# Kernel tuning notes

Measured on AMD Instinct MI355X. Metric: run time of the kernel, lower is better.

Reference implementation:

```python
import jax, jax.numpy as jnp
import numpy as np

N, B, H, IN_DIM, OUT_DIM = 1024, 16, 64, 2, 12
BACK, STEP = 2.0, 1.0
HIST = int(BACK / STEP)          # history steps = 2
FUR = int(OUT_DIM / STEP)        # future integration steps = 12
THRES = 1e-3                     # edge threshold (thres in __init__)
NBINS = HIST + 1                 # quantized delay bins: 0..HIST steps
N_KNOTS = 11                     # spline intervals (12 knots)


def setup_inputs() -> dict:
    key = jax.random.key(0)
    ks = iter(jax.random.split(key, 32))
    f32 = jnp.float32

    def rn(shape, scale):
        return (scale * jax.random.normal(next(ks), shape, dtype=f32))

    inp = {
        "A": jax.random.uniform(next(ks), (N, N), dtype=f32),
        "all_delay": jax.random.uniform(next(ks), (N, N), dtype=f32) * BACK,
        "coeff_a": rn((B, N, N_KNOTS, IN_DIM), 0.1),
        "coeff_b": rn((B, N, N_KNOTS, IN_DIM), 0.1),
        "coeff_c": rn((B, N, N_KNOTS, IN_DIM), 0.1),
        "coeff_d": rn((B, N, N_KNOTS, IN_DIM), 0.1),
        "node_emb": rn((N, H), 0.1),
        "i2h_W1": rn((IN_DIM, H), 1.0 / np.sqrt(IN_DIM)),
        "i2h_b1": jnp.zeros((H,), f32),
        "i2h_W2": rn((H, H * HIST), 1.0 / np.sqrt(H)),
        "i2h_b2": jnp.zeros((H * HIST,), f32),
        "dde_Wm": rn((H, H), 1.0 / np.sqrt(H)),
        "dde_Ws": rn((H, H), 1.0 / np.sqrt(H)),
        "dde_Wx": rn((IN_DIM, H), 1.0 / np.sqrt(IN_DIM)),
        "dde_b": jnp.zeros((H,), f32),
        "reg_W1": rn((H, H // 2), 1.0 / np.sqrt(H)),
        "reg_b1": jnp.zeros((H // 2,), f32),
        "reg_W2": rn((H // 2, 1), 1.0 / np.sqrt(H // 2)),
        "reg_b2": jnp.zeros((1,), f32),
        "pred_W1": rn((H, H // 2), 1.0 / np.sqrt(H)),
        "pred_b1": jnp.zeros((H // 2,), f32),
        "pred_W2": rn((H // 2, OUT_DIM), 1.0 / np.sqrt(H // 2)),
        "pred_b2": jnp.zeros((OUT_DIM,), f32),
    }
    return inp


def _spline(coeffs, t):
    """Natural cubic spline: value and derivative at scalar time t.
    knots at times BACK + arange(12); coeffs [B,N,11,IN]."""
    a, b, c, d = coeffs
    idx = jnp.clip(jnp.floor(t - BACK).astype(jnp.int32), 0, a.shape[2] - 1)
    frac = t - BACK - idx.astype(a.dtype)
    A_ = jnp.take(a, idx, axis=2)
    B_ = jnp.take(b, idx, axis=2)
    C_ = jnp.take(c, idx, axis=2)
    D_ = jnp.take(d, idx, axis=2)
    val = A_ + frac * (B_ + frac * (C_ + frac * D_))
    der = B_ + frac * (2.0 * C_ + 3.0 * frac * D_)
    return val, der  # each [B,N,IN]


def _forward(A, all_delay, coeff_a, coeff_b, coeff_c, coeff_d, node_emb,
             i2h_W1, i2h_b1, i2h_W2, i2h_b2,
             dde_Wm, dde_Ws, dde_Wx, dde_b,
             reg_W1, reg_b1, reg_W2, reg_b2,
             pred_W1, pred_b1, pred_W2, pred_b2):
    coeffs = (coeff_a, coeff_b, coeff_c, coeff_d)
    # --- dynamic graph build (dense, thresholded) ---
    sem = jax.nn.softmax(jax.nn.relu(node_emb @ node_emb.T), axis=1)     # semantic_A
    Ah = A + jnp.eye(N, dtype=A.dtype)                                   # normalized adj
    dinv = jax.lax.rsqrt(Ah.sum(axis=1))
    spatial = dinv[:, None] * Ah * dinv[None, :]
    Ac = sem + spatial
    W = jnp.where(Ac > THRES, Ac, 0.0)                                   # edge weights
    dsteps = jnp.round(jnp.clip(all_delay, 0.0, BACK) / STEP).astype(jnp.int32)
    Wbins = jnp.stack([jnp.where(dsteps == d, W, 0.0) for d in range(NBINS)])  # [NBINS,N,N]

    # --- history hidden states from initial spline value ---
    x0, _ = _spline(coeffs, jnp.asarray(BACK, A.dtype))                  # [B,N,IN]
    hid = jax.nn.relu(x0 @ i2h_W1 + i2h_b1) @ i2h_W2 + i2h_b2            # [B,N,H*HIST]
    hist = hid.reshape(B, N, HIST, H).transpose(1, 2, 0, 3)              # [N,HIST,B,H]
    S = jnp.concatenate([hist, jnp.zeros((N, FUR, B, H), hist.dtype)], axis=1)
    h0 = hist[:, HIST - 1]                                               # y0 [N,B,H]

    def step(carry, k):
        S, h = carry
        idx = HIST - 1 + k  # current time index in S
        agg = jnp.zeros_like(h)
        for d in range(NBINS):  # delayed message passing per delay bin
            sd = jax.lax.dynamic_slice_in_dim(S, jnp.maximum(idx - d, 0), 1, axis=1)[:, 0]
            agg = agg + jnp.einsum('ji,jbh->ibh', Wbins[d], sd)
        t = BACK + STEP * k.astype(h.dtype)
        _, dx = _spline(coeffs, t)                                       # control derivative
        dx = dx.transpose(1, 0, 2)                                       # [N,B,IN]
        pre = agg @ dde_Wm + h @ dde_Ws + dx @ dde_Wx + dde_b
        h_new = h + STEP * (jnp.tanh(pre) - h)                           # Euler step of DDE
        S = jax.lax.dynamic_update_slice_in_dim(S, h_new[:, None], idx + 1, axis=1)
        return (S, h_new), h_new

    (_, _), y_hidden = jax.lax.scan(step, (S, h0), jnp.arange(FUR))      # [FUR,N,B,H]

    reg = (jax.nn.relu(y_hidden @ reg_W1 + reg_b1) @ reg_W2 + reg_b2)[..., 0]  # [FUR,N,B]
    ts = BACK + jnp.arange(OUT_DIM, dtype=A.dtype)
    tgt = jax.vmap(lambda t: _spline(coeffs, t)[0][:, :, 0].T)(ts)       # [OUT,N,B]
    diff = reg - tgt
    ad = jnp.abs(diff)
    reg_loss = jnp.where(ad < 1.0, 0.5 * diff * diff, ad - 0.5).mean()

    y_pred = (jax.nn.relu(y_hidden[-1] @ pred_W1 + pred_b1) @ pred_W2 + pred_b2)
    y_pred = y_pred.transpose(1, 0, 2)                                   # [B,N,OUT]
    return y_pred, reg_loss


def reference(A, all_delay, coeff_a, coeff_b, coeff_c, coeff_d, node_emb,
              i2h_W1, i2h_b1, i2h_W2, i2h_b2,
              dde_Wm, dde_Ws, dde_Wx, dde_b,
              reg_W1, reg_b1, reg_W2, reg_b2,
              pred_W1, pred_b1, pred_W2, pred_b2):
    return _forward(A, all_delay, coeff_a, coeff_b, coeff_c, coeff_d, node_emb,
                    i2h_W1, i2h_b1, i2h_W2, i2h_b2,
                    dde_Wm, dde_Ws, dde_Wx, dde_b,
                    reg_W1, reg_b1, reg_W2, reg_b2,
                    pred_W1, pred_b1, pred_W2, pred_b2)
```

## Files before the change

kernel.cpp:

```cpp
#include <hip/hip_runtime.h>
#include <cstddef>
#include <cstdint>

#define NN 1024
#define BB 16
#define NKNOTS 11

typedef __attribute__((ext_vector_type(8))) short short8_v;
typedef __attribute__((ext_vector_type(4))) float f32x4;
typedef __attribute__((ext_vector_type(8))) unsigned short ushort8_v;
typedef __attribute__((ext_vector_type(4))) unsigned short ushort4_v;
typedef __attribute__((ext_vector_type(4))) unsigned int uint4_v;
typedef __attribute__((ext_vector_type(2))) unsigned int uint2_v;

#define WPK_OFF   ((size_t)0)
#define M3_OFF    ((size_t)2 << 20)
#define STHI_OFF  ((size_t)6 << 20)
#define STLO_OFF  ((size_t)14 << 20)
#define WGT_OFF   ((size_t)22 << 20)
#define SYNC_OFF  (((size_t)22 << 20) + 16384)
#define LOSS_OFF  (SYNC_OFF + 2048)
#define Z_OFF     (LOSS_OFF + 256)
#define DINV_OFF  (Z_OFF + 4096)

#define AGGS   0
#define AGGH   17408
#define AGGL   25600
#define HH_    33792
#define HL_    41984
#define HT32   50176
#define REDS   66560
#define PL1    68608
#define WGT_L  104448
#define LUT_OFF 120832

__device__ __forceinline__ unsigned short f2bf(float x) {
  unsigned int u = __float_as_uint(x);
  return (unsigned short)((u + 0x7FFFu + ((u >> 16) & 1u)) >> 16);
}
__device__ __forceinline__ float bf2f(unsigned short h) {
  return __uint_as_float(((unsigned int)h) << 16);
}
__device__ __forceinline__ void gload16(const void* g, void* l) {
  __builtin_amdgcn_global_load_lds(
      (const __attribute__((address_space(1))) unsigned int*)g,
      (__attribute__((address_space(3))) unsigned int*)l, 16, 0, 0);
}
__device__ __forceinline__ void gload4(const void* g, void* l) {
  __builtin_amdgcn_global_load_lds(
      (const __attribute__((address_space(1))) unsigned int*)g,
      (__attribute__((address_space(3))) unsigned int*)l, 4, 0, 0);
}

__global__ __launch_bounds__(256) void rowstats_kernel(
    const float* __restrict__ emb, const float* __restrict__ A,
    float* __restrict__ Z, float* __restrict__ dinv)
{
  const int j = blockIdx.x;
  const int tid = threadIdx.x;
  __shared__ float ej[64];
  __shared__ float r1[256], r2[256];
  if (tid < 64) ej[tid] = emb[j * 64 + tid];
  __syncthreads();
  float zs = 0.f, as = 0.f;
  for (int i = tid; i < NN; i += 256) {
    const float4* er = (const float4*)(emb + (size_t)i * 64);
    float dot = 0.f;
#pragma unroll
    for (int q = 0; q < 16; ++q) {
      float4 e = er[q];
      dot += e.x * ej[q * 4 + 0] + e.y * ej[q * 4 + 1] +
             e.z * ej[q * 4 + 2] + e.w * ej[q * 4 + 3];
    }
    zs += expf(fmaxf(dot, 0.f));
    as += A[(size_t)j * NN + i];
  }
  r1[tid] = zs; r2[tid] = as;
  __syncthreads();
  for (int s = 128; s > 0; s >>= 1) {
    if (tid < s) { r1[tid] += r1[tid + s]; r2[tid] += r2[tid + s]; }
    __syncthreads();
  }
  if (tid == 0) {
    Z[j] = r1[0];
    dinv[j] = rsqrtf(r2[0] + 1.0f);
  }
}

__global__ __launch_bounds__(256) void build_wt_kernel(
    const float* __restrict__ emb, const float* __restrict__ A,
    const float* __restrict__ delay, const float* __restrict__ Z,
    const float* __restrict__ dinv,
    unsigned short* __restrict__ Wpk, unsigned int* __restrict__ M3g)
{
  __shared__ float eI[64][65];
  __shared__ float eJ[64][65];
  __shared__ float wS[64][65];
  __shared__ unsigned char dS[64][64];
  __shared__ float diS[64];

  const int tid = threadIdx.x;
  const int it = blockIdx.x >> 4, jt = blockIdx.x & 15;
  const int i0 = it * 64, j0 = jt * 64;

  for (int q = tid; q < 4096; q += 256) {
    int r = q >> 6, c = q & 63;
    eI[r][c] = emb[(size_t)(i0 + r) * 64 + c];
    eJ[r][c] = emb[(size_t)(j0 + r) * 64 + c];
  }
  if (tid < 64) diS[tid] = dinv[i0 + tid];
  __syncthreads();

  const int jj = tid >> 2, iig = (tid & 3) * 16;
  float dotv[16];
#pragma unroll
  for (int m = 0; m < 16; ++m) dotv[m] = 0.f;
#pragma unroll 4
  for (int h4 = 0; h4 < 16; ++h4) {
    float4 a = *(const float4*)&eJ[jj][h4 * 4];
#pragma unroll
    for (int m = 0; m < 16; ++m) {
      float4 bb = *(const float4*)&eI[iig + m][h4 * 4];
      dotv[m] += a.x * bb.x + a.y * bb.y + a.z * bb.z + a.w * bb.w;
    }
  }
  const float Zj = Z[j0 + jj], dj = dinv[j0 + jj];
  const float* Ap = A + (size_t)(j0 + jj) * NN + i0 + iig;
  const float* Dp = delay + (size_t)(j0 + jj) * NN + i0 + iig;
#pragma unroll
  for (int m = 0; m < 16; ++m) {
    float aji = Ap[m] + ((i0 + iig + m) == (j0 + jj) ? 1.f : 0.f);
    float ac = expf(fmaxf(dotv[m], 0.f)) / Zj + dj * diS[iig + m] * aji;
    float w = (ac > 0.001f) ? ac : 0.f;
    float dl = fminf(fmaxf(Dp[m], 0.f), 2.f);
    wS[jj][iig + m] = w;
    dS[jj][iig + m] = (unsigned char)(int)rintf(dl);
  }
  __syncthreads();

  const int iw = tid >> 2, jg = (tid & 3) * 16;
  ushort8_v P0, P1;
#pragma unroll
  for (int m = 0; m < 8; ++m) {
    P0[m] = f2bf(wS[jg + m][iw]);
    P1[m] = f2bf(wS[jg + 8 + m][iw]);
  }
  size_t woff = (size_t)(i0 + iw) * NN + j0 + jg;
  *(ushort8_v*)(Wpk + woff) = P0;
  *(ushort8_v*)(Wpk + woff + 8) = P1;
  uint2_v mw;
#pragma unroll
  for (int o = 0; o < 2; ++o) {
    unsigned int m0 = 0, m1 = 0, m2 = 0;
#pragma unroll
    for (int e = 0; e < 8; ++e) {
      int dv = dS[jg + o * 8 + e][iw];
      m0 |= (dv == 0) << e;
      m1 |= (dv == 1) << e;
      m2 |= (dv == 2) << e;
    }
    mw[o] = m0 | (m1 << 8) | (m2 << 16);
  }
  *(uint2_v*)(M3g + (size_t)(i0 + iw) * 128 + (j0 + jg) / 8) = mw;
}

__global__ __launch_bounds__(256) void init_s_kernel(
    const float* __restrict__ ca, const float* __restrict__ W1,
    const float* __restrict__ b1, const float* __restrict__ W2,
    const float* __restrict__ b2,
    unsigned short* __restrict__ SThi, unsigned short* __restrict__ STlo,
    const float* __restrict__ Wm, const float* __restrict__ Wsm,
    unsigned short* __restrict__ wgt)
{
  const int bid = blockIdx.x;
  const int tid = threadIdx.x;
  if (bid >= 256) {
    int e = (bid - 256) * 256 + tid;
    int n = e >> 7, kk = e & 127;
    float v = (kk < 64) ? Wm[kk * 64 + n] : Wsm[(kk - 64) * 64 + n];
    wgt[n * 128 + (((kk >> 3) ^ (n & 15)) << 3) + (kk & 7)] = f2bf(v);
    return;
  }
  __shared__ float l1S[64][65];
  __shared__ float W2S[64][128];
  __shared__ float hidS[64][129];

  const int nt = bid >> 4, b = bid & 15;
  const int n0 = nt * 64;

  for (int q = tid; q < 2048; q += 256)
    ((float4*)&W2S[0][0])[q] = ((const float4*)W2)[q];

  {
    const int n = tid >> 2, hb = (tid & 3) * 16;
    float2 x = *(const float2*)(ca + ((size_t)(b * NN + n0 + n) * NKNOTS) * 2);
#pragma unroll
    for (int m = 0; m < 16; ++m) {
      int h = hb + m;
      l1S[n][h] = fmaxf(x.x * W1[h] + x.y * W1[64 + h] + b1[h], 0.f);
    }
  }
  __syncthreads();
  {
    const int nn = tid & 63, o0 = (tid >> 6) * 32;
    float hid[32];
#pragma unroll
    for (int o = 0; o < 32; ++o) hid[o] = b2[o0 + o];
    for (int h = 0; h < 64; ++h) {
      float lv = l1S[nn][h];
#pragma unroll
      for (int o = 0; o < 32; ++o) hid[o] = fmaf(lv, W2S[h][o0 + o], hid[o]);
    }
#pragma unroll
    for (int o = 0; o < 32; ++o) hidS[nn][o0 + o] = hid[o];
  }
  __syncthreads();
  {
    const int r = tid >> 1, hf = tid & 1;
    const int t = r >> 6, hh = r & 63;
    size_t off = ((size_t)t << 20) + (size_t)(b * 64 + hh) * NN + n0 + hf * 32;
    ushort8_v H[4], L[4];
#pragma unroll
    for (int q = 0; q < 4; ++q)
#pragma unroll
      for (int m = 0; m < 8; ++m) {
        float v = hidS[hf * 32 + q * 8 + m][r];
        unsigned short hv = f2bf(v);
        H[q][m] = hv; L[q][m] = f2bf(v - bf2f(hv));
      }
#pragma unroll
    for (int q = 0; q < 4; ++q) {
      *(ushort8_v*)(SThi + off + q * 8) = H[q];
      *(ushort8_v*)(STlo + off + q * 8) = L[q];
    }
  }
}

__global__ __launch_bounds__(512, 2) void scan_kernel(
    const unsigned short* __restrict__ Wpk, const unsigned int* __restrict__ M3g,
    unsigned short* __restrict__ SThi, unsigned short* __restrict__ STlo,
    const unsigned short* __restrict__ wgt, unsigned int* __restrict__ syncc,
    const float* __restrict__ Wx, const float* __restrict__ db,
    const float* __restrict__ cb, const float* __restrict__ cc,
    const float* __restrict__ cd, const float* __restrict__ ca,
    const float* __restrict__ rW1, const float* __restrict__ rb1,
    const float* __restrict__ rW2, const float* __restrict__ rb2,
    const float* __restrict__ pW1, const float* __restrict__ pb1,
    const float* __restrict__ pW2, const float* __restrict__ pb2,
    float* __restrict__ out, float* __restrict__ loss)
{
  __shared__ __align__(16) char smem[120960];
  __shared__ float sWx[128];
  __shared__ float sdb[64];

  const int tid  = threadIdx.x;
  const int lane = tid & 63;
  const int w    = tid >> 6;
  const int bid  = blockIdx.x;
  const int i_t = bid >> 4;
  const int b   = bid & 15;
  const int i0 = i_t * 64, c0 = b * 64;

  const int wr = (w >> 1) & 1, wc = w & 1, kh = w >> 2;
  const int g = lane >> 4, l15 = lane & 15;

  if (tid < 128) sWx[tid] = Wx[tid];
  else if (tid < 192) sdb[tid - 128] = db[tid - 128];

  if (tid < 32) {
    int n = tid >> 1, half = tid & 1;
    unsigned int dw = half == 0
      ? (((n & 1) ? 0xFFFFu : 0u) | ((n & 2) ? 0xFFFF0000u : 0u))
      : (((n & 4) ? 0xFFFFu : 0u) | ((n & 8) ? 0xFFFF0000u : 0u));
    *(unsigned int*)(smem + LUT_OFF + n * 8 + half * 4) = dw;
  }

  gload16(wgt + (size_t)tid * 8,        smem + WGT_L + tid * 16);
  gload16(wgt + 4096 + (size_t)tid * 8, smem + WGT_L + 8192 + tid * 16);
  __syncthreads();

  const int s_row = tid >> 3;
  const int s_ch  = tid & 7;
  const int s_cx  = (s_ch ^ (s_row & 7)) * 8;
  const int koff  = kh * 4 + g;
  const int s16   = (koff ^ (l15 & 7)) << 4;
  const int rowA0 = wr * 32 + l15;
  const int rB0   = 10240 + (wc * 32 + l15) * 128 + s16;

  float (*aggS)[68] = (float (*)[68])(smem + AGGS);

  for (int k = 0; k < 12; ++k) {
    f32x4 acc[2][2];
#pragma unroll
    for (int fr = 0; fr < 2; ++fr)
#pragma unroll
      for (int fc = 0; fc < 2; ++fc)
        acc[fr][fc] = (f32x4){0.f, 0.f, 0.f, 0.f};

    auto stage = [&](int t) {
      const int jc = t << 6;
      char* dst = smem + (t % 3) * 34816;
      gload16(Wpk + (size_t)(i0 + s_row) * NN + jc + s_cx, dst + tid * 16);
      gload4(M3g + (size_t)(i0 + s_row) * 128 + (jc >> 3) + s_ch,
             dst + 8192 + tid * 4);
#pragma unroll
      for (int d = 0; d < 3; ++d) {
        int td = k + 1 - d; if (td < 0) td = 0;
        gload16(SThi + ((size_t)(td & 3) << 20) +
                    (size_t)(c0 + s_row) * NN + jc + s_cx,
                dst + 10240 + d * 8192 + tid * 16);
      }
    };

    stage(0); stage(1);
    asm volatile("s_waitcnt vmcnt(5)" ::: "memory");
    __builtin_amdgcn_s_barrier();

    for (int t = 0; t < 16; ++t) {
      if (t < 14) stage(t + 2);
      const char* bp = smem + (t % 3) * 34816;
      short8_v w0 = *(const short8_v*)(bp + rowA0 * 128 + s16);
      short8_v w1 = *(const short8_v*)(bp + (rowA0 + 16) * 128 + s16);
      unsigned int m0 = *(const unsigned int*)(bp + 8192 + rowA0 * 32 + koff * 4);
      unsigned int m1 = *(const unsigned int*)(bp + 8192 + (rowA0 + 16) * 32 + koff * 4);
#pragma unroll
      for (int d = 0; d < 3; ++d) {
        unsigned int mb0 = (m0 >> (8 * d)) & 0xFF;
        unsigned int mb1 = (m1 >> (8 * d)) & 0xFF;
        uint2_v lo0 = *(const uint2_v*)(smem + LUT_OFF + (mb0 & 15) * 8);
        uint2_v hi0 = *(const uint2_v*)(smem + LUT_OFF + (mb0 >> 4) * 8);
        uint2_v lo1 = *(const uint2_v*)(smem + LUT_OFF + (mb1 & 15) * 8);
        uint2_v hi1 = *(const uint2_v*)(smem + LUT_OFF + (mb1 >> 4) * 8);
        short8_v a0 = w0, a1 = w1;
        unsigned int* a0p = (unsigned int*)&a0;
        unsigned int* a1p = (unsigned int*)&a1;
        a0p[0] &= lo0[0]; a0p[1] &= lo0[1]; a0p[2] &= hi0[0]; a0p[3] &= hi0[1];
        a1p[0] &= lo1[0]; a1p[1] &= lo1[1]; a1p[2] &= hi1[0]; a1p[3] &= hi1[1];
        short8_v b0 = *(const short8_v*)(bp + d * 8192 + rB0);
        short8_v b1 = *(const short8_v*)(bp + d * 8192 + rB0 + 16 * 128);
        acc[0][0] = __builtin_amdgcn_mfma_f32_16x16x32_bf16(a0, b0, acc[0][0], 0, 0, 0);
        acc[0][1] = __builtin_amdgcn_mfma_f32_16x16x32_bf16(a0, b1, acc[0][1], 0, 0, 0);
        acc[1][0] = __builtin_amdgcn_mfma_f32_16x16x32_bf16(a1, b0, acc[1][0], 0, 0, 0);
        acc[1][1] = __builtin_amdgcn_mfma_f32_16x16x32_bf16(a1, b1, acc[1][1], 0, 0, 0);
      }
      __builtin_amdgcn_sched_barrier(0);
      if (t < 14) {
        asm volatile("s_waitcnt vmcnt(5)" ::: "memory");
        __builtin_amdgcn_s_barrier();
      } else if (t == 14) {
        asm volatile("s_waitcnt vmcnt(0)" ::: "memory");
        __builtin_amdgcn_s_barrier();
      }
    }
    __syncthreads();

    if (kh == 0) {
#pragma unroll
      for (int fr = 0; fr < 2; ++fr)
#pragma unroll
        for (int fc = 0; fc < 2; ++fc)
#pragma unroll
          for (int rr = 0; rr < 4; ++rr)
            aggS[wr * 32 + fr * 16 + g * 4 + rr][wc * 32 + fc * 16 + l15] = acc[fr][fc][rr];
    }
    __syncthreads();
    if (kh == 1) {
#pragma unroll
      for (int fr = 0; fr < 2; ++fr)
#pragma unroll
        for (int fc = 0; fc < 2; ++fc)
#pragma unroll
          for (int rr = 0; rr < 4; ++rr)
            aggS[wr * 32 + fr * 16 + g * 4 + rr][wc * 32 + fc * 16 + l15] += acc[fr][fc][rr];
    }
    __syncthreads();

    {
      const int row = tid >> 3, c8 = tid & 7;
      const float* src = &aggS[row][c8 * 8];
      ushort8_v H, L;
#pragma unroll
      for (int q = 0; q < 8; ++q) {
        float f = src[q];
        unsigned short hv = f2bf(f);
        H[q] = hv; L[q] = f2bf(f - bf2f(hv));
      }
      const int pos = (c8 ^ (row & 7)) << 4;
      *(ushort8_v*)(smem + AGGH + row * 128 + pos) = H;
      *(ushort8_v*)(smem + AGGL + row * 128 + pos) = L;
    }
    {
      const int cl = tid >> 3, ich = (tid & 7) * 8;
      size_t off = ((size_t)((k + 1) & 3) << 20) + (size_t)(c0 + cl) * NN + (i0 + ich);
      ushort8_v h8 = *(const ushort8_v*)(SThi + off);
      ushort8_v l8 = *(const ushort8_v*)(STlo + off);
#pragma unroll
      for (int q = 0; q < 8; ++q) {
        int i = ich + q;
        int byo = i * 128 + ((((cl >> 3) ^ (i & 7))) << 4) + (cl & 7) * 2;
        *(unsigned short*)(smem + HH_ + byo) = h8[q];
        *(unsigned short*)(smem + HL_ + byo) = l8[q];
      }
    }
    __syncthreads();

    const int mr = w & 3, nc = w >> 2;
    f32x4 pacc[2];
    pacc[0] = (f32x4){0.f, 0.f, 0.f, 0.f};
    pacc[1] = (f32x4){0.f, 0.f, 0.f, 0.f};
#pragma unroll
    for (int ks = 0; ks < 4; ++ks) {
      const int base = (ks < 2) ? AGGH : HH_;
      const int ks2 = ks & 1;
      const int cxa = ((ks2 * 4 + g) ^ (l15 & 7)) << 4;
      const char* ra = smem + base + (mr * 16 + l15) * 128 + cxa;
      short8_v aH = *(const short8_v*)ra;
      short8_v aL = *(const short8_v*)(ra + 8192);
#pragma unroll
      for (int fc = 0; fc < 2; ++fc) {
        const int n = (nc * 2 + fc) * 16 + l15;
        const int cxb = ((ks * 4 + g) ^ l15) << 4;
        short8_v bv = *(const short8_v*)(smem + WGT_L + n * 256 + cxb);
        pacc[fc] = __builtin_amdgcn_mfma_f32_16x16x32_bf16(aH, bv, pacc[fc], 0, 0, 0);
        pacc[fc] = __builtin_amdgcn_mfma_f32_16x16x32_bf16(aL, bv, pacc[fc], 0, 0, 0);
      }
    }
    __syncthreads();

    const int ksp = (k < 11) ? k : 10;
    float hn[2][4];
#pragma unroll
    for (int rr = 0; rr < 4; ++rr) {
      int iG = i0 + mr * 16 + g * 4 + rr;
      size_t cbase = ((size_t)(b * NN + iG) * NKNOTS + ksp) * 2;
      float dx0 = cb[cbase + 0], dx1 = cb[cbase + 1];
      if (k == 11) {
        dx0 += 2.f * cc[cbase + 0] + 3.f * cd[cbase + 0];
        dx1 += 2.f * cc[cbase + 1] + 3.f * cd[cbase + 1];
      }
#pragma unroll
      for (int fc = 0; fc < 2; ++fc) {
        int hcol = (nc * 2 + fc) * 16 + l15;
        float pre = pacc[fc][rr] + dx0 * sWx[hcol] + dx1 * sWx[64 + hcol] + sdb[hcol];
        hn[fc][rr] = tanhf(pre);
      }
    }
#pragma unroll
    for (int fc = 0; fc < 2; ++fc) {
      int hcol = (nc * 2 + fc) * 16 + l15;
      int iG0 = i0 + mr * 16 + g * 4;
      size_t off2 = ((size_t)((k + 2) & 3) << 20) + (size_t)(c0 + hcol) * NN + iG0;
      ushort4_v H4, L4;
      uint4_v pk;
#pragma unroll
      for (int rr = 0; rr < 4; ++rr) {
        unsigned short hv = f2bf(hn[fc][rr]);
        unsigned short lv = f2bf(hn[fc][rr] - bf2f(hv));
        H4[rr] = hv; L4[rr] = lv;
        pk[rr] = ((unsigned int)hv << 16) | lv;
      }
      *(ushort4_v*)(SThi + off2) = H4;
      *(ushort4_v*)(STlo + off2) = L4;
      const int ci = mr * 4 + g;
      *(uint4_v*)(smem + HT32 + hcol * 256 + ((ci ^ (hcol & 15)) << 4)) = pk;
    }
    asm volatile("s_waitcnt vmcnt(0)" ::: "memory");
    __syncthreads();
    if (tid == 0) atomicAdd(&syncc[b * 32 + k], 1u);

    {
      const int ii = tid & 63, mg4 = (tid >> 6) * 4;
      float s0 = rb1[mg4], s1 = rb1[mg4 + 1], s2 = rb1[mg4 + 2], s3 = rb1[mg4 + 3];
#pragma unroll 8
      for (int h = 0; h < 64; ++h) {
        unsigned int v = *(const unsigned int*)(smem + HT32 + h * 256 +
                           ((((ii >> 2) ^ (h & 15))) << 4) + (ii & 3) * 4);
        float f = bf2f((unsigned short)(v >> 16)) + bf2f((unsigned short)(v & 0xffff));
        float4 wv = *(const float4*)(rW1 + h * 32 + mg4);
        s0 = fmaf(f, wv.x, s0); s1 = fmaf(f, wv.y, s1);
        s2 = fmaf(f, wv.z, s2); s3 = fmaf(f, wv.w, s3);
      }
      float4 r2v = *(const float4*)(rW2 + mg4);
      float rp = fmaxf(s0, 0.f) * r2v.x + fmaxf(s1, 0.f) * r2v.y +
                 fmaxf(s2, 0.f) * r2v.z + fmaxf(s3, 0.f) * r2v.w;
      float* redS = (float*)(smem + REDS);
      redS[(tid >> 6) * 64 + ii] = rp;
      __syncthreads();
      if (tid < 64) {
        float rv = rb2[0];
#pragma unroll
        for (int m = 0; m < 8; ++m) rv += redS[m * 64 + tid];
        int iG = i0 + tid;
        size_t tb = ((size_t)(b * NN + iG) * NKNOTS + ksp) * 2;
        float tgt = ca[tb];
        if (k == 11) tgt += cb[tb] + cc[tb] + cd[tb];
        float dv = rv - tgt;
        float ad = fabsf(dv);
        float hub = (ad < 1.f) ? 0.5f * dv * dv : (ad - 0.5f);
        hub += __shfl_down(hub, 32);
        hub += __shfl_down(hub, 16);
        hub += __shfl_down(hub, 8);
        hub += __shfl_down(hub, 4);
        hub += __shfl_down(hub, 2);
        hub += __shfl_down(hub, 1);
        if (tid == 0) atomicAdd(loss, hub);
      }
    }

    if (k == 11) {
      __syncthreads();
      const int ii = tid & 63, mg4 = (tid >> 6) * 4;
      float s0 = pb1[mg4], s1 = pb1[mg4 + 1], s2 = pb1[mg4 + 2], s3 = pb1[mg4 + 3];
#pragma unroll 8
      for (int h = 0; h < 64; ++h) {
        unsigned int v = *(const unsigned int*)(smem + HT32 + h * 256 +
                           ((((ii >> 2) ^ (h & 15))) << 4) + (ii & 3) * 4);
        float f = bf2f((unsigned short)(v >> 16)) + bf2f((unsigned short)(v & 0xffff));
        float4 wv = *(const float4*)(pW1 + h * 32 + mg4);
        s0 = fmaf(f, wv.x, s0); s1 = fmaf(f, wv.y, s1);
        s2 = fmaf(f, wv.z, s2); s3 = fmaf(f, wv.w, s3);
      }
      float* pl1 = (float*)(smem + PL1);
      pl1[ii * 32 + mg4 + 0] = fmaxf(s0, 0.f);
      pl1[ii * 32 + mg4 + 1] = fmaxf(s1, 0.f);
      pl1[ii * 32 + mg4 + 2] = fmaxf(s2, 0.f);
      pl1[ii * 32 + mg4 + 3] = fmaxf(s3, 0.f);
      __syncthreads();
#pragma unroll
      for (int rep = 0; rep < 2; ++rep) {
        int idxp = tid + rep * 512;
        if (idxp < 768) {
          int i_ = idxp / 12, o = idxp % 12;
          float s = pb2[o];
#pragma unroll
          for (int m = 0; m < 32; ++m) s = fmaf(pl1[i_ * 32 + m], pW2[m * 12 + o], s);
          out[((size_t)b * NN + (i0 + i_)) * 12 + o] = s;
        }
      }
    }

    __syncthreads();
    if (tid == 0) {
      unsigned int* ctr = &syncc[b * 32 + k];
      while (atomicAdd(ctr, 0u) < 16u) __builtin_amdgcn_s_sleep(1);
      asm volatile("buffer_inv sc0" ::: "memory");
    }
    __syncthreads();
  }
}

__global__ void finalize_kernel(const float* __restrict__ loss, float* __restrict__ out)
{
  out[196608] = loss[0] * (1.0f / 196608.0f);
}

extern "C" void kernel_launch(void* const* d_in, const int* in_sizes, int n_in,
                              void* d_out, int out_size, void* d_ws, size_t ws_size,
                              hipStream_t stream)
{
  const float* A     = (const float*)d_in[0];
  const float* delay = (const float*)d_in[1];
  const float* ca    = (const float*)d_in[2];
  const float* cb    = (const float*)d_in[3];
  const float* cc    = (const float*)d_in[4];
  const float* cd    = (const float*)d_in[5];
  const float* emb   = (const float*)d_in[6];
  const float* iW1   = (const float*)d_in[7];
  const float* ib1   = (const float*)d_in[8];
  const float* iW2   = (const float*)d_in[9];
  const float* ib2   = (const float*)d_in[10];
  const float* Wm    = (const float*)d_in[11];
  const float* Wsm   = (const float*)d_in[12];
  const float* Wx    = (const float*)d_in[13];
  const float* db    = (const float*)d_in[14];
  const float* rW1   = (const float*)d_in[15];
  const float* rb1   = (const float*)d_in[16];
  const float* rW2   = (const float*)d_in[17];
  const float* rb2   = (const float*)d_in[18];
  const float* pW1   = (const float*)d_in[19];
  const float* pb1   = (const float*)d_in[20];
  const float* pW2   = (const float*)d_in[21];
  const float* pb2   = (const float*)d_in[22];

  char* wsb = (char*)d_ws;
  float* out = (float*)d_out;
  unsigned short* Wpk  = (unsigned short*)(wsb + WPK_OFF);
  unsigned int*  M3g   = (unsigned int*)(wsb + M3_OFF);
  unsigned short* SThi = (unsigned short*)(wsb + STHI_OFF);
  unsigned short* STlo = (unsigned short*)(wsb + STLO_OFF);
  unsigned short* wgt  = (unsigned short*)(wsb + WGT_OFF);
  unsigned int* syncc  = (unsigned int*)(wsb + SYNC_OFF);
  float* loss          = (float*)(wsb + LOSS_OFF);
  float* Z             = (float*)(wsb + Z_OFF);
  float* dinv          = (float*)(wsb + DINV_OFF);

  hipMemsetAsync(syncc, 0, 2048 + 64, stream);
  rowstats_kernel<<<NN, 256, 0, stream>>>(emb, A, Z, dinv);
  build_wt_kernel<<<256, 256, 0, stream>>>(emb, A, delay, Z, dinv, Wpk, M3g);
  init_s_kernel<<<288, 256, 0, stream>>>(ca, iW1, ib1, iW2, ib2,
                                         SThi, STlo, Wm, Wsm, wgt);
  scan_kernel<<<256, 512, 0, stream>>>(
      Wpk, M3g, SThi, STlo, wgt, syncc, Wx, db, cb, cc, cd, ca,
      rW1, rb1, rW2, rb2, pW1, pb1, pW2, pb2, out, loss);
  finalize_kernel<<<1, 1, 0, stream>>>(loss, out);
}
```

Measured before the change: 391.7 us.

## Halve scan row tile to 32 and launch 512 blocks with register-loaded W

After: 606.0 us. 1.55x slower.

```diff
diff --git a/kernel.cpp b/kernel.cpp
--- a/kernel.cpp
+++ b/kernel.cpp
@@ -24,15 +24,14 @@
 #define DINV_OFF  (Z_OFF + 4096)
 
 #define AGGS   0
-#define AGGH   17408
-#define AGGL   25600
-#define HH_    33792
-#define HL_    41984
-#define HT32   50176
-#define REDS   66560
-#define PL1    68608
-#define WGT_L  104448
-#define LUT_OFF 120832
+#define AGGH   8704
+#define AGGL   12800
+#define HH_    16896
+#define HL_    20992
+#define HT32   25088
+#define REDS   33280
+#define PL1    35328
+#define LUT_OFF 73728
 
 __device__ __forceinline__ unsigned short f2bf(float x) {
   unsigned int u = __float_as_uint(x);
@@ -45,11 +44,6 @@
   __builtin_amdgcn_global_load_lds(
       (const __attribute__((address_space(1))) unsigned int*)g,
       (__attribute__((address_space(3))) unsigned int*)l, 16, 0, 0);
-}
-__device__ __forceinline__ void gload4(const void* g, void* l) {
-  __builtin_amdgcn_global_load_lds(
-      (const __attribute__((address_space(1))) unsigned int*)g,
-      (__attribute__((address_space(3))) unsigned int*)l, 4, 0, 0);
 }
 
 __global__ __launch_bounds__(256) void rowstats_kernel(
@@ -178,7 +172,7 @@
     int e = (bid - 256) * 256 + tid;
     int n = e >> 7, kk = e & 127;
     float v = (kk < 64) ? Wm[kk * 64 + n] : Wsm[(kk - 64) * 64 + n];
-    wgt[n * 128 + (((kk >> 3) ^ (n & 15)) << 3) + (kk & 7)] = f2bf(v);
+    wgt[n * 128 + kk] = f2bf(v);
     return;
   }
   __shared__ float l1S[64][65];
@@ -236,7 +230,7 @@
   }
 }
 
-__global__ __launch_bounds__(512, 2) void scan_kernel(
+__global__ __launch_bounds__(512, 4) void scan_kernel(
     const unsigned short* __restrict__ Wpk, const unsigned int* __restrict__ M3g,
     unsigned short* __restrict__ SThi, unsigned short* __restrict__ STlo,
     const unsigned short* __restrict__ wgt, unsigned int* __restrict__ syncc,
@@ -249,7 +243,7 @@
     const float* __restrict__ pW2, const float* __restrict__ pb2,
     float* __restrict__ out, float* __restrict__ loss)
 {
-  __shared__ __align__(16) char smem[120960];
+  __shared__ __align__(16) char smem[73856];
   __shared__ float sWx[128];
   __shared__ float sdb[64];
 
@@ -259,9 +253,9 @@
   const int bid  = blockIdx.x;
   const int i_t = bid >> 4;
   const int b   = bid & 15;
-  const int i0 = i_t * 64, c0 = b * 64;
-
-  const int wr = (w >> 1) & 1, wc = w & 1, kh = w >> 2;
+  const int i0 = i_t * 32, c0 = b * 64;
+
+  const int fr = w & 1, wc = (w >> 1) & 1, kh = w >> 2;
   const int g = lane >> 4, l15 = lane & 15;
 
   if (tid < 128) sWx[tid] = Wx[tid];
@@ -274,108 +268,94 @@
       : (((n & 4) ? 0xFFFFu : 0u) | ((n & 8) ? 0xFFFF0000u : 0u));
     *(unsigned int*)(smem + LUT_OFF + n * 8 + half * 4) = dw;
   }
-
-  gload16(wgt + (size_t)tid * 8,        smem + WGT_L + tid * 16);
-  gload16(wgt + 4096 + (size_t)tid * 8, smem + WGT_L + 8192 + tid * 16);
   __syncthreads();
 
   const int s_row = tid >> 3;
   const int s_ch  = tid & 7;
   const int s_cx  = (s_ch ^ (s_row & 7)) * 8;
-  const int koff  = kh * 4 + g;
-  const int s16   = (koff ^ (l15 & 7)) << 4;
-  const int rowA0 = wr * 32 + l15;
-  const int rB0   = 10240 + (wc * 32 + l15) * 128 + s16;
+  const int koff = kh * 4 + g;
+  const int s16  = (koff ^ (l15 & 7)) << 4;
+  const int rB0  = (wc * 32 + l15) * 128 + s16;
+  const unsigned short* Wrow = Wpk + (size_t)(i0 + fr * 16 + l15) * NN + koff * 8;
+  const unsigned int*   Mrow = M3g + (size_t)(i0 + fr * 16 + l15) * 128 + koff;
 
   float (*aggS)[68] = (float (*)[68])(smem + AGGS);
 
   for (int k = 0; k < 12; ++k) {
-    f32x4 acc[2][2];
-#pragma unroll
-    for (int fr = 0; fr < 2; ++fr)
-#pragma unroll
-      for (int fc = 0; fc < 2; ++fc)
-        acc[fr][fc] = (f32x4){0.f, 0.f, 0.f, 0.f};
+    f32x4 acc[2];
+    acc[0] = (f32x4){0.f, 0.f, 0.f, 0.f};
+    acc[1] = (f32x4){0.f, 0.f, 0.f, 0.f};
 
     auto stage = [&](int t) {
       const int jc = t << 6;
-      char* dst = smem + (t % 3) * 34816;
-      gload16(Wpk + (size_t)(i0 + s_row) * NN + jc + s_cx, dst + tid * 16);
-      gload4(M3g + (size_t)(i0 + s_row) * 128 + (jc >> 3) + s_ch,
-             dst + 8192 + tid * 4);
+      char* dst = smem + (t % 3) * 24576;
 #pragma unroll
       for (int d = 0; d < 3; ++d) {
         int td = k + 1 - d; if (td < 0) td = 0;
         gload16(SThi + ((size_t)(td & 3) << 20) +
                     (size_t)(c0 + s_row) * NN + jc + s_cx,
-                dst + 10240 + d * 8192 + tid * 16);
+                dst + d * 8192 + tid * 16);
       }
     };
 
+    short8_v wv_c, wv_n;
+    unsigned int wm_c, wm_n;
+    wv_c = *(const short8_v*)(Wrow);
+    wm_c = Mrow[0];
     stage(0); stage(1);
-    asm volatile("s_waitcnt vmcnt(5)" ::: "memory");
+    asm volatile("s_waitcnt vmcnt(3)" ::: "memory");
     __builtin_amdgcn_s_barrier();
 
     for (int t = 0; t < 16; ++t) {
+      if (t < 15) {
+        wv_n = *(const short8_v*)(Wrow + (t + 1) * 64);
+        wm_n = Mrow[(t + 1) * 8];
+      }
       if (t < 14) stage(t + 2);
-      const char* bp = smem + (t % 3) * 34816;
-      short8_v w0 = *(const short8_v*)(bp + rowA0 * 128 + s16);
-      short8_v w1 = *(const short8_v*)(bp + (rowA0 + 16) * 128 + s16);
-      unsigned int m0 = *(const unsigned int*)(bp + 8192 + rowA0 * 32 + koff * 4);
-      unsigned int m1 = *(const unsigned int*)(bp + 8192 + (rowA0 + 16) * 32 + koff * 4);
+      const char* bp = smem + (t % 3) * 24576;
 #pragma unroll
       for (int d = 0; d < 3; ++d) {
-        unsigned int mb0 = (m0 >> (8 * d)) & 0xFF;
-        unsigned int mb1 = (m1 >> (8 * d)) & 0xFF;
-        uint2_v lo0 = *(const uint2_v*)(smem + LUT_OFF + (mb0 & 15) * 8);
-        uint2_v hi0 = *(const uint2_v*)(smem + LUT_OFF + (mb0 >> 4) * 8);
-        uint2_v lo1 = *(const uint2_v*)(smem + LUT_OFF + (mb1 & 15) * 8);
-        uint2_v hi1 = *(const uint2_v*)(smem + LUT_OFF + (mb1 >> 4) * 8);
-        short8_v a0 = w0, a1 = w1;
-        unsigned int* a0p = (unsigned int*)&a0;
-        unsigned int* a1p = (unsigned int*)&a1;
-        a0p[0] &= lo0[0]; a0p[1] &= lo0[1]; a0p[2] &= hi0[0]; a0p[3] &= hi0[1];
-        a1p[0] &= lo1[0]; a1p[1] &= lo1[1]; a1p[2] &= hi1[0]; a1p[3] &= hi1[1];
+        unsigned int mb = (wm_c >> (8 * d)) & 0xFF;
+        uint2_v lo = *(const uint2_v*)(smem + LUT_OFF + (mb & 15) * 8);
+        uint2_v hi = *(const uint2_v*)(smem + LUT_OFF + (mb >> 4) * 8);
+        short8_v a = wv_c;
+        unsigned int* ap = (unsigned int*)&a;
+        ap[0] &= lo[0]; ap[1] &= lo[1]; ap[2] &= hi[0]; ap[3] &= hi[1];
         short8_v b0 = *(const short8_v*)(bp + d * 8192 + rB0);
-        short8_v b1 = *(const short8_v*)(bp + d * 8192 + rB0 + 16 * 128);
-        acc[0][0] = __builtin_amdgcn_mfma_f32_16x16x32_bf16(a0, b0, acc[0][0], 0, 0, 0);
-        acc[0][1] = __builtin_amdgcn_mfma_f32_16x16x32_bf16(a0, b1, acc[0][1], 0, 0, 0);
-        acc[1][0] = __builtin_amdgcn_mfma_f32_16x16x32_bf16(a1, b0, acc[1][0], 0, 0, 0);
-        acc[1][1] = __builtin_amdgcn_mfma_f32_16x16x32_bf16(a1, b1, acc[1][1], 0, 0, 0);
+        short8_v b1 = *(const short8_v*)(bp + d * 8192 + rB0 + 2048);
+        acc[0] = __builtin_amdgcn_mfma_f32_16x16x32_bf16(a, b0, acc[0], 0, 0, 0);
+        acc[1] = __builtin_amdgcn_mfma_f32_16x16x32_bf16(a, b1, acc[1], 0, 0, 0);
       }
       __builtin_amdgcn_sched_barrier(0);
       if (t < 14) {
-        asm volatile("s_waitcnt vmcnt(5)" ::: "memory");
+        asm volatile("s_waitcnt vmcnt(3)" ::: "memory");
         __builtin_amdgcn_s_barrier();
       } else if (t == 14) {
         asm volatile("s_waitcnt vmcnt(0)" ::: "memory");
         __builtin_amdgcn_s_barrier();
       }
+      wv_c = wv_n; wm_c = wm_n;
     }
     __syncthreads();
 
     if (kh == 0) {
 #pragma unroll
-      for (int fr = 0; fr < 2; ++fr)
-#pragma unroll
-        for (int fc = 0; fc < 2; ++fc)
-#pragma unroll
-          for (int rr = 0; rr < 4; ++rr)
-            aggS[wr * 32 + fr * 16 + g * 4 + rr][wc * 32 + fc * 16 + l15] = acc[fr][fc][rr];
+      for (int fc = 0; fc < 2; ++fc)
+#pragma unroll
+        for (int rr = 0; rr < 4; ++rr)
+          aggS[fr * 16 + g * 4 + rr][wc * 32 + fc * 16 + l15] = acc[fc][rr];
     }
     __syncthreads();
     if (kh == 1) {
 #pragma unroll
-      for (int fr = 0; fr < 2; ++fr)
-#pragma unroll
-        for (int fc = 0; fc < 2; ++fc)
-#pragma unroll
-          for (int rr = 0; rr < 4; ++rr)
-            aggS[wr * 32 + fr * 16 + g * 4 + rr][wc * 32 + fc * 16 + l15] += acc[fr][fc][rr];
-    }
-    __syncthreads();
-
-    {
+      for (int fc = 0; fc < 2; ++fc)
+#pragma unroll
+        for (int rr = 0; rr < 4; ++rr)
+          aggS[fr * 16 + g * 4 + rr][wc * 32 + fc * 16 + l15] += acc[fc][rr];
+    }
+    __syncthreads();
+
+    if (tid < 256) {
       const int row = tid >> 3, c8 = tid & 7;
       const float* src = &aggS[row][c8 * 8];
       ushort8_v H, L;
@@ -388,9 +368,9 @@
       const int pos = (c8 ^ (row & 7)) << 4;
       *(ushort8_v*)(smem + AGGH + row * 128 + pos) = H;
       *(ushort8_v*)(smem + AGGL + row * 128 + pos) = L;
-    }
-    {
-      const int cl = tid >> 3, ich = (tid & 7) * 8;
+    } else {
+      const int t2 = tid - 256;
+      const int cl = t2 >> 2, ich = (t2 & 3) * 8;
       size_t off = ((size_t)((k + 1) & 3) << 20) + (size_t)(c0 + cl) * NN + (i0 + ich);
       ushort8_v h8 = *(const ushort8_v*)(SThi + off);
       ushort8_v l8 = *(const ushort8_v*)(STlo + off);
@@ -404,31 +384,24 @@
     }
     __syncthreads();
 
-    const int mr = w & 3, nc = w >> 2;
-    f32x4 pacc[2];
-    pacc[0] = (f32x4){0.f, 0.f, 0.f, 0.f};
-    pacc[1] = (f32x4){0.f, 0.f, 0.f, 0.f};
+    const int mr = w & 1, nc = w >> 1;
+    f32x4 pacc = (f32x4){0.f, 0.f, 0.f, 0.f};
 #pragma unroll
     for (int ks = 0; ks < 4; ++ks) {
       const int base = (ks < 2) ? AGGH : HH_;
-      const int ks2 = ks & 1;
-      const int cxa = ((ks2 * 4 + g) ^ (l15 & 7)) << 4;
+      const int cxa = (((ks & 1) * 4 + g) ^ (l15 & 7)) << 4;
       const char* ra = smem + base + (mr * 16 + l15) * 128 + cxa;
       short8_v aH = *(const short8_v*)ra;
-      short8_v aL = *(const short8_v*)(ra + 8192);
-#pragma unroll
-      for (int fc = 0; fc < 2; ++fc) {
-        const int n = (nc * 2 + fc) * 16 + l15;
-        const int cxb = ((ks * 4 + g) ^ l15) << 4;
-        short8_v bv = *(const short8_v*)(smem + WGT_L + n * 256 + cxb);
-        pacc[fc] = __builtin_amdgcn_mfma_f32_16x16x32_bf16(aH, bv, pacc[fc], 0, 0, 0);
-        pacc[fc] = __builtin_amdgcn_mfma_f32_16x16x32_bf16(aL, bv, pacc[fc], 0, 0, 0);
-      }
+      short8_v aL = *(const short8_v*)(ra + 4096);
+      short8_v bv = *(const short8_v*)(wgt + (size_t)(nc * 16 + l15) * 128 + (ks * 4 + g) * 8);
+      pacc = __builtin_amdgcn_mfma_f32_16x16x32_bf16(aH, bv, pacc, 0, 0, 0);
+      pacc = __builtin_amdgcn_mfma_f32_16x16x32_bf16(aL, bv, pacc, 0, 0, 0);
     }
     __syncthreads();
 
     const int ksp = (k < 11) ? k : 10;
-    float hn[2][4];
+    float hn[4];
+    const int hcol = nc * 16 + l15;
 #pragma unroll
     for (int rr = 0; rr < 4; ++rr) {
       int iG = i0 + mr * 16 + g * 4 + rr;
@@ -438,58 +411,54 @@
         dx0 += 2.f * cc[cbase + 0] + 3.f * cd[cbase + 0];
         dx1 += 2.f * cc[cbase + 1] + 3.f * cd[cbase + 1];
       }
-#pragma unroll
-      for (int fc = 0; fc < 2; ++fc) {
-        int hcol = (nc * 2 + fc) * 16 + l15;
-        float pre = pacc[fc][rr] + dx0 * sWx[hcol] + dx1 * sWx[64 + hcol] + sdb[hcol];
-        hn[fc][rr] = tanhf(pre);
-      }
-    }
-#pragma unroll
-    for (int fc = 0; fc < 2; ++fc) {
-      int hcol = (nc * 2 + fc) * 16 + l15;
+      float pre = pacc[rr] + dx0 * sWx[hcol] + dx1 * sWx[64 + hcol] + sdb[hcol];
+      hn[rr] = tanhf(pre);
+    }
+    {
       int iG0 = i0 + mr * 16 + g * 4;
       size_t off2 = ((size_t)((k + 2) & 3) << 20) + (size_t)(c0 + hcol) * NN + iG0;
       ushort4_v H4, L4;
       uint4_v pk;
 #pragma unroll
       for (int rr = 0; rr < 4; ++rr) {
-        unsigned short hv = f2bf(hn[fc][rr]);
-        unsigned short lv = f2bf(hn[fc][rr] - bf2f(hv));
+        unsigned short hv = f2bf(hn[rr]);
+        unsigned short lv = f2bf(hn[rr] - bf2f(hv));
         H4[rr] = hv; L4[rr] = lv;
         pk[rr] = ((unsigned int)hv << 16) | lv;
       }
       *(ushort4_v*)(SThi + off2) = H4;
       *(ushort4_v*)(STlo + off2) = L4;
       const int ci = mr * 4 + g;
-      *(uint4_v*)(smem + HT32 + hcol * 256 + ((ci ^ (hcol & 15)) << 4)) = pk;
+      *(uint4_v*)(smem + HT32 + hcol * 128 + ((ci ^ (hcol & 7)) << 4)) = pk;
     }
     asm volatile("s_waitcnt vmcnt(0)" ::: "memory");
     __syncthreads();
     if (tid == 0) atomicAdd(&syncc[b * 32 + k], 1u);
 
     {
-      const int ii = tid & 63, mg4 = (tid >> 6) * 4;
-      float s0 = rb1[mg4], s1 = rb1[mg4 + 1], s2 = rb1[mg4 + 2], s3 = rb1[mg4 + 3];
+      float* redS = (float*)(smem + REDS);
+      if (tid < 256) {
+        const int ii = tid & 31, mg4 = (tid >> 5) * 4;
+        float s0 = rb1[mg4], s1 = rb1[mg4 + 1], s2 = rb1[mg4 + 2], s3 = rb1[mg4 + 3];
 #pragma unroll 8
-      for (int h = 0; h < 64; ++h) {
-        unsigned int v = *(const unsigned int*)(smem + HT32 + h * 256 +
-                           ((((ii >> 2) ^ (h & 15))) << 4) + (ii & 3) * 4);
-        float f = bf2f((unsigned short)(v >> 16)) + bf2f((unsigned short)(v & 0xffff));
-        float4 wv = *(const float4*)(rW1 + h * 32 + mg4);
-        s0 = fmaf(f, wv.x, s0); s1 = fmaf(f, wv.y, s1);
-        s2 = fmaf(f, wv.z, s2); s3 = fmaf(f, wv.w, s3);
-      }
-      float4 r2v = *(const float4*)(rW2 + mg4);
-      float rp = fmaxf(s0, 0.f) * r2v.x + fmaxf(s1, 0.f) * r2v.y +
-                 fmaxf(s2, 0.f) * r2v.z + fmaxf(s3, 0.f) * r2v.w;
-      float* redS = (float*)(smem + REDS);
-      redS[(tid >> 6) * 64 + ii] = rp;
+        for (int h = 0; h < 64; ++h) {
+          unsigned int v = *(const unsigned int*)(smem + HT32 + h * 128 +
+                             ((((ii >> 2) ^ (h & 7))) << 4) + (ii & 3) * 4);
+          float f = bf2f((unsigned short)(v >> 16)) + bf2f((unsigned short)(v & 0xffff));
+          float4 wv = *(const float4*)(rW1 + h * 32 + mg4);
+          s0 = fmaf(f, wv.x, s0); s1 = fmaf(f, wv.y, s1);
+          s2 = fmaf(f, wv.z, s2); s3 = fmaf(f, wv.w, s3);
+        }
+        float4 r2v = *(const float4*)(rW2 + mg4);
+        float rp = fmaxf(s0, 0.f) * r2v.x + fmaxf(s1, 0.f) * r2v.y +
+                   fmaxf(s2, 0.f) * r2v.z + fmaxf(s3, 0.f) * r2v.w;
+        redS[(tid >> 5) * 32 + ii] = rp;
+      }
       __syncthreads();
-      if (tid < 64) {
+      if (tid < 32) {
         float rv = rb2[0];
 #pragma unroll
-        for (int m = 0; m < 8; ++m) rv += redS[m * 64 + tid];
+        for (int m = 0; m < 8; ++m) rv += redS[m * 32 + tid];
         int iG = i0 + tid;
         size_t tb = ((size_t)(b * NN + iG) * NKNOTS + ksp) * 2;
         float tgt = ca[tb];
@@ -497,7 +466,6 @@
         float dv = rv - tgt;
         float ad = fabsf(dv);
         float hub = (ad < 1.f) ? 0.5f * dv * dv : (ad - 0.5f);
-        hub += __shfl_down(hub, 32);
         hub += __shfl_down(hub, 16);
         hub += __shfl_down(hub, 8);
         hub += __shfl_down(hub, 4);
@@ -509,40 +477,39 @@
 
     if (k == 11) {
       __syncthreads();
-      const int ii = tid & 63, mg4 = (tid >> 6) * 4;
-      float s0 = pb1[mg4], s1 = pb1[mg4 + 1], s2 = pb1[mg4 + 2], s3 = pb1[mg4 + 3];
+      if (tid < 256) {
+        const int ii = tid & 31, mg4 = (tid >> 5) * 4;
+        float s0 = pb1[mg4], s1 = pb1[mg4 + 1], s2 = pb1[mg4 + 2], s3 = pb1[mg4 + 3];
 #pragma unroll 8
-      for (int h = 0; h < 64; ++h) {
-        unsigned int v = *(const unsigned int*)(smem + HT32 + h * 256 +
-                           ((((ii >> 2) ^ (h & 15))) << 4) + (ii & 3) * 4);
-        float f = bf2f((unsigned short)(v >> 16)) + bf2f((unsigned short)(v & 0xffff));
-        float4 wv = *(const float4*)(pW1 + h * 32 + mg4);
-        s0 = fmaf(f, wv.x, s0); s1 = fmaf(f, wv.y, s1);
-        s2 = fmaf(f, wv.z, s2); s3 = fmaf(f, wv.w, s3);
-      }
-      float* pl1 = (float*)(smem + PL1);
-      pl1[ii * 32 + mg4 + 0] = fmaxf(s0, 0.f);
-      pl1[ii * 32 + mg4 + 1] = fmaxf(s1, 0.f);
-      pl1[ii * 32 + mg4 + 2] = fmaxf(s2, 0.f);
-      pl1[ii * 32 + mg4 + 3] = fmaxf(s3, 0.f);
+        for (int h = 0; h < 64; ++h) {
+          unsigned int v = *(const unsigned int*)(smem + HT32 + h * 128 +
+                             ((((ii >> 2) ^ (h & 7))) << 4) + (ii & 3) * 4);
+          float f = bf2f((unsigned short)(v >> 16)) + bf2f((unsigned short)(v & 0xffff));
+          float4 wv = *(const float4*)(pW1 + h * 32 + mg4);
+          s0 = fmaf(f, wv.x, s0); s1 = fmaf(f, wv.y, s1);
+          s2 = fmaf(f, wv.z, s2); s3 = fmaf(f, wv.w, s3);
+        }
+        float* pl1 = (float*)(smem + PL1);
+        pl1[ii * 32 + mg4 + 0] = fmaxf(s0, 0.f);
+        pl1[ii * 32 + mg4 + 1] = fmaxf(s1, 0.f);
+        pl1[ii * 32 + mg4 + 2] = fmaxf(s2, 0.f);
+        pl1[ii * 32 + mg4 + 3] = fmaxf(s3, 0.f);
+      }
       __syncthreads();
-#pragma unroll
-      for (int rep = 0; rep < 2; ++rep) {
-        int idxp = tid + rep * 512;
-        if (idxp < 768) {
-          int i_ = idxp / 12, o = idxp % 12;
-          float s = pb2[o];
-#pragma unroll
-          for (int m = 0; m < 32; ++m) s = fmaf(pl1[i_ * 32 + m], pW2[m * 12 + o], s);
-          out[((size_t)b * NN + (i0 + i_)) * 12 + o] = s;
-        }
+      if (tid < 384) {
+        float* pl1 = (float*)(smem + PL1);
+        int i_ = tid / 12, o = tid % 12;
+        float s = pb2[o];
+#pragma unroll
+        for (int m = 0; m < 32; ++m) s = fmaf(pl1[i_ * 32 + m], pW2[m * 12 + o], s);
+        out[((size_t)b * NN + (i0 + i_)) * 12 + o] = s;
       }
     }
 
     __syncthreads();
     if (tid == 0) {
       unsigned int* ctr = &syncc[b * 32 + k];
-      while (atomicAdd(ctr, 0u) < 16u) __builtin_amdgcn_s_sleep(1);
+      while (atomicAdd(ctr, 0u) < 32u) __builtin_amdgcn_s_sleep(1);
       asm volatile("buffer_inv sc0" ::: "memory");
     }
     __syncthreads();
@@ -599,7 +566,7 @@
   build_wt_kernel<<<256, 256, 0, stream>>>(emb, A, delay, Z, dinv, Wpk, M3g);
   init_s_kernel<<<288, 256, 0, stream>>>(ca, iW1, ib1, iW2, ib2,
                                          SThi, STlo, Wm, Wsm, wgt);
-  scan_kernel<<<256, 512, 0, stream>>>(
+  scan_kernel<<<512, 512, 0, stream>>>(
       Wpk, M3g, SThi, STlo, wgt, syncc, Wx, db, cb, cc, cd, ca,
       rW1, rb1, rW2, rb2, pW1, pb1, pW2, pb2, out, loss);
   finalize_kernel<<<1, 1, 0, stream>>>(loss, out);
```
